# Kernel tuning notes

Measured on AMD Instinct MI355X. Metric: run time of the kernel, lower is better.

## Reference

```python
import jax, jax.numpy as jnp
import numpy as np


def _knn_idx(pts, k):
    # pts: [N, d] -> indices of k nearest neighbors (incl. self, loop=True) [N, k]
    sq = jnp.sum(pts * pts, axis=-1)
    d2 = sq[:, None] + sq[None, :] - 2.0 * (pts @ pts.T)  # [N, N] squared dists
    _, idx = jax.lax.top_k(-d2, k)  # k smallest distances
    return idx


def _graph_conv(x, nbr, Wr, br, Ws):
    # x: [B, N, d_in], nbr: [B, N, k]. GraphConv (aggr='add'):
    # out_i = W_rel @ sum_j x_j + b_rel + W_root @ x_i
    gathered = jax.vmap(lambda xb, ib: xb[ib])(x, nbr)  # [B, N, k, d_in]
    agg = gathered.sum(axis=2)                          # [B, N, d_in]
    return agg @ Wr.T + br + x @ Ws.T


def setup_inputs() -> dict:
    key = jax.random.key(0)
    ks = jax.random.split(key, 10)
    B, N, D, H = 16, 2048, 3, 128
    s = lambda fi, fo: (2.0 / (fi + fo)) ** 0.5
    return {
        "point_cloud": jax.random.normal(ks[0], (B, N, D), dtype=jnp.float32),
        "W1r": jax.random.normal(ks[1], (H, D), dtype=jnp.float32) * s(D, H),
        "b1": jnp.zeros((H,), dtype=jnp.float32),
        "W1s": jax.random.normal(ks[2], (H, D), dtype=jnp.float32) * s(D, H),
        "W2r": jax.random.normal(ks[3], (H, H), dtype=jnp.float32) * s(H, H),
        "b2": jnp.zeros((H,), dtype=jnp.float32),
        "W2s": jax.random.normal(ks[4], (H, H), dtype=jnp.float32) * s(H, H),
        "W3r": jax.random.normal(ks[5], (H, H), dtype=jnp.float32) * s(H, H),
        "b3": jnp.zeros((H,), dtype=jnp.float32),
        "W3s": jax.random.normal(ks[6], (H, H), dtype=jnp.float32) * s(H, H),
        "k": 16,
    }


def reference(point_cloud, W1r, b1, W1s, W2r, b2, W2s, W3r, b3, W3s, k):
    # knn graph per batch element (loop=True: self-loop included, d(i,i)=0)
    nbr = jax.vmap(lambda p: _knn_idx(p, k))(point_cloud)  # [B, N, k]
    x = jax.nn.relu(_graph_conv(point_cloud, nbr, W1r, b1, W1s))
    x = jax.nn.relu(_graph_conv(x, nbr, W2r, b2, W2s))
    x = _graph_conv(x, nbr, W3r, b3, W3s)
    return x  # [B, N, output_dim]
```

## Files before the change

kernel.cpp:

```cpp
#include <hip/hip_runtime.h>
#include <math.h>

#define NPTS 2048
#define BATCH 16
#define KNN 16
#define HID 128
#define RPB 8
#define CAP 128

typedef __attribute__((ext_vector_type(8))) short bf16x8;
typedef __attribute__((ext_vector_type(4))) float f32x4;

__device__ inline unsigned short f2bf(float f) {
    unsigned u = __float_as_uint(f);
    return (unsigned short)((u + 0x7FFFu + ((u >> 16) & 1u)) >> 16);
}
__device__ inline float bflo(unsigned v) { return __uint_as_float(v << 16); }
__device__ inline float bfhi(unsigned v) { return __uint_as_float(v & 0xFFFF0000u); }

__global__ __launch_bounds__(512) void knn_kernel(
    const float* __restrict__ pc, int* __restrict__ nbr,
    const float* __restrict__ W1r, const float* __restrict__ b1,
    const float* __restrict__ W1s, unsigned short* __restrict__ x1)
{
    __shared__ __align__(16) float4 pts[NPTS];
    __shared__ unsigned ckey[RPB][CAP];
    __shared__ unsigned cidx[RPB][CAP];

    const int b = blockIdx.x >> 8;
    const int rblk = blockIdx.x & 255;
    const float* p = pc + (size_t)b * NPTS * 3;

    for (int t = threadIdx.x; t < NPTS; t += 512) {
        float x = p[t * 3 + 0], y = p[t * 3 + 1], z = p[t * 3 + 2];
        pts[t] = make_float4(x, y, z, x * x + y * y + z * z);
    }
    __syncthreads();

    const int w = threadIdx.x >> 6;
    const int lane = threadIdx.x & 63;
    const int i = rblk * RPB + w;
    const float4 pi = pts[i];
    const float piw16 = pi.w + 16.0f;

    unsigned key[32];
    unsigned km = 0xFFFFFFFFu;
    #pragma unroll
    for (int t = 0; t < 32; ++t) {
        float4 c = pts[t * 64 + lane];
        float dot = fmaf(pi.x, c.x, fmaf(pi.y, c.y, pi.z * c.z));
        float d2 = fmaf(-2.0f, dot, piw16 + c.w);
        key[t] = __float_as_uint(d2);
        km = min(km, key[t]);
    }

    unsigned v = km;
    #pragma unroll
    for (int k = 2; k <= 64; k <<= 1) {
        #pragma unroll
        for (int j = k >> 1; j > 0; j >>= 1) {
            unsigned o = (unsigned)__shfl_xor((int)v, j, 64);
            bool sel = ((lane & k) == 0) == ((lane & j) == 0);
            v = sel ? min(v, o) : max(v, o);
        }
    }
    const unsigned T0 = (unsigned)__shfl((int)v, 15, 64);

    unsigned base = 0;
    #pragma unroll 1
    for (int t = 0; t < 32; ++t) {
        bool pred = key[t] <= T0;
        unsigned long long mask = __ballot(pred);
        if (mask) {
            unsigned prefix = __builtin_amdgcn_mbcnt_hi(
                (unsigned)(mask >> 32),
                __builtin_amdgcn_mbcnt_lo((unsigned)mask, 0));
            unsigned pos = base + prefix;
            if (pred && pos < CAP) {
                ckey[w][pos] = key[t];
                cidx[w][pos] = (unsigned)(t * 64 + lane);
            }
            base += (unsigned)__popcll(mask);
        }
    }
    __threadfence_block();
    const int m = (int)base;

    int* out = nbr + ((size_t)b * NPTS + i) * KNN;
    float ax = 0.f, ay = 0.f, az = 0.f;

    if (m <= CAP) {
        unsigned k0 = (lane < m) ? ckey[w][lane] : 0xFFFFFFFFu;
        unsigned k1 = (lane + 64 < m) ? ckey[w][lane + 64] : 0xFFFFFFFFu;
        int r0 = 0, r1 = 0;
        if (m <= 64) {
            #pragma unroll 1
            for (int jj = 0; jj < m; ++jj) {
                unsigned kj = ckey[w][jj];
                r0 += (kj < k0) || (kj == k0 && jj < lane);
            }
        } else {
            #pragma unroll 1
            for (int jj = 0; jj < m; ++jj) {
                unsigned kj = ckey[w][jj];
                r0 += (kj < k0) || (kj == k0 && jj < lane);
                r1 += (kj < k1) || (kj == k1 && jj < lane + 64);
            }
        }
        if (lane < m && r0 < KNN) {
            unsigned j = cidx[w][lane];
            out[r0] = (int)j;
            float4 q = pts[j]; ax += q.x; ay += q.y; az += q.z;
        }
        if (m > 64 && lane + 64 < m && r1 < KNN) {
            unsigned j = cidx[w][lane + 64];
            out[r1] = (int)j;
            float4 q = pts[j]; ax += q.x; ay += q.y; az += q.z;
        }
    } else {
        unsigned T = 0;
        #pragma unroll 1
        for (int bit = 31; bit >= 0; --bit) {
            unsigned trial = T | (1u << bit);
            int cnt = 0;
            #pragma unroll
            for (int t = 0; t < 32; ++t) cnt += (key[t] < trial);
            #pragma unroll
            for (int off = 32; off; off >>= 1)
                cnt += __shfl_xor(cnt, off, 64);
            if (cnt < KNN) T = trial;
        }
        unsigned bs = 0;
        #pragma unroll 1
        for (int t = 0; t < 32; ++t) {
            bool p1 = key[t] < T;
            unsigned long long mask = __ballot(p1);
            if (mask) {
                unsigned prefix = __builtin_amdgcn_mbcnt_hi(
                    (unsigned)(mask >> 32),
                    __builtin_amdgcn_mbcnt_lo((unsigned)mask, 0));
                if (p1) {
                    out[bs + prefix] = t * 64 + lane;
                    float4 q = pts[t * 64 + lane];
                    ax += q.x; ay += q.y; az += q.z;
                }
                bs += (unsigned)__popcll(mask);
            }
        }
        #pragma unroll 1
        for (int t = 0; t < 32 && bs < KNN; ++t) {
            bool p2 = key[t] == T;
            unsigned long long mask = __ballot(p2);
            if (mask) {
                unsigned prefix = __builtin_amdgcn_mbcnt_hi(
                    (unsigned)(mask >> 32),
                    __builtin_amdgcn_mbcnt_lo((unsigned)mask, 0));
                unsigned pos = bs + prefix;
                if (p2 && pos < KNN) {
                    out[pos] = t * 64 + lane;
                    float4 q = pts[t * 64 + lane];
                    ax += q.x; ay += q.y; az += q.z;
                }
                bs += (unsigned)__popcll(mask);
            }
        }
    }

    #pragma unroll
    for (int off = 32; off; off >>= 1) {
        ax += __shfl_xor(ax, off, 64);
        ay += __shfl_xor(ay, off, 64);
        az += __shfl_xor(az, off, 64);
    }

    unsigned short* xrow = x1 + ((size_t)b * NPTS + i) * HID;
    #pragma unroll
    for (int hh = 0; hh < 2; ++hh) {
        int h = lane + hh * 64;
        float acc = b1[h];
        acc += W1r[h * 3 + 0] * ax + W1r[h * 3 + 1] * ay + W1r[h * 3 + 2] * az;
        acc += W1s[h * 3 + 0] * pi.x + W1s[h * 3 + 1] * pi.y + W1s[h * 3 + 2] * pi.z;
        xrow[h] = f2bf(fmaxf(acc, 0.f));
    }
}

__global__ __launch_bounds__(256) void wcvt_kernel(
    const float* __restrict__ a, const float* __restrict__ b,
    const float* __restrict__ c, const float* __restrict__ d,
    unsigned short* __restrict__ out)
{
    int g = blockIdx.x * 256 + threadIdx.x;
    int m = g >> 14;
    const float* s = (m == 0) ? a : (m == 1) ? b : (m == 2) ? c : d;
    out[g] = f2bf(s[g & 16383]);
}

template <bool RELU, bool OUT_BF16>
__global__ __launch_bounds__(1024, 8) void conv_fused(
    const unsigned short* __restrict__ x, const int* __restrict__ nbr,
    const unsigned short* __restrict__ Wr, const unsigned short* __restrict__ Ws,
    const float* __restrict__ bias, void* __restrict__ outv)
{
    __shared__ __align__(16) unsigned short aggs[64][136];
    __shared__ int nbrs[64][17];
    const int p0 = blockIdx.x * 64;
    const int bt = p0 >> 11;
    const unsigned short* xb = x + ((size_t)bt << 11) * HID;

    {
        int e = threadIdx.x;
        nbrs[e >> 4][e & 15] = nbr[(size_t)p0 * KNN + e];
    }
    __syncthreads();

    {
        int c8 = threadIdx.x & 15, pt = threadIdx.x >> 4;
        const unsigned short* base = xb + c8 * 8;
        float s[8] = {0, 0, 0, 0, 0, 0, 0, 0};
        #pragma unroll
        for (int t = 0; t < KNN; ++t) {
            int j = nbrs[pt][t];
            uint4 v = *(const uint4*)(base + (size_t)j * HID);
            s[0] += bflo(v.x); s[1] += bfhi(v.x);
            s[2] += bflo(v.y); s[3] += bfhi(v.y);
            s[4] += bflo(v.z); s[5] += bfhi(v.z);
            s[6] += bflo(v.w); s[7] += bfhi(v.w);
        }
        uint4 ov;
        ov.x = (unsigned)f2bf(s[0]) | ((unsigned)f2bf(s[1]) << 16);
        ov.y = (unsigned)f2bf(s[2]) | ((unsigned)f2bf(s[3]) << 16);
        ov.z = (unsigned)f2bf(s[4]) | ((unsigned)f2bf(s[5]) << 16);
        ov.w = (unsigned)f2bf(s[6]) | ((unsigned)f2bf(s[7]) << 16);
        *(uint4*)&aggs[pt][c8 * 8] = ov;
    }
    __syncthreads();

    const int wv = threadIdx.x >> 6;
    const int lane = threadIdx.x & 63;
    const int ptw = (wv & 3) * 16;
    const int h0w = (wv >> 2) * 32;
    const int row = lane & 15;
    const int quad = lane >> 4;

    f32x4 acc[2];
    acc[0] = (f32x4){0, 0, 0, 0};
    acc[1] = (f32x4){0, 0, 0, 0};

    #pragma unroll
    for (int kc = 0; kc < 4; ++kc) {
        bf16x8 a0 = *(const bf16x8*)&aggs[ptw + row][quad * 8 + kc * 32];
        #pragma unroll
        for (int n = 0; n < 2; ++n) {
            bf16x8 bb = *(const bf16x8*)&Wr[(size_t)(h0w + n * 16 + row) * HID
                                            + quad * 8 + kc * 32];
            acc[n] = __builtin_amdgcn_mfma_f32_16x16x32_bf16(a0, bb, acc[n], 0, 0, 0);
        }
    }
    const unsigned short* xr0 = x + (size_t)(p0 + ptw + row) * HID + quad * 8;
    #pragma unroll
    for (int kc = 0; kc < 4; ++kc) {
        bf16x8 a0 = *(const bf16x8*)(xr0 + kc * 32);
        #pragma unroll
        for (int n = 0; n < 2; ++n) {
            bf16x8 bb = *(const bf16x8*)&Ws[(size_t)(h0w + n * 16 + row) * HID
                                            + quad * 8 + kc * 32];
            acc[n] = __builtin_amdgcn_mfma_f32_16x16x32_bf16(a0, bb, acc[n], 0, 0, 0);
        }
    }

    #pragma unroll
    for (int n = 0; n < 2; ++n) {
        float bh = bias[h0w + n * 16 + row];
        #pragma unroll
        for (int r = 0; r < 4; ++r) {
            int pp = p0 + ptw + quad * 4 + r;
            float vv = acc[n][r] + bh;
            if (RELU) vv = fmaxf(vv, 0.f);
            if (OUT_BF16)
                ((unsigned short*)outv)[(size_t)pp * HID + h0w + n * 16 + row] = f2bf(vv);
            else
                ((float*)outv)[(size_t)pp * HID + h0w + n * 16 + row] = vv;
        }
    }
}

extern "C" void kernel_launch(void* const* d_in, const int* in_sizes, int n_in,
                              void* d_out, int out_size, void* d_ws, size_t ws_size,
                              hipStream_t stream)
{
    const float* pc  = (const float*)d_in[0];
    const float* W1r = (const float*)d_in[1];
    const float* b1  = (const float*)d_in[2];
    const float* W1s = (const float*)d_in[3];
    const float* W2r = (const float*)d_in[4];
    const float* b2  = (const float*)d_in[5];
    const float* W2s = (const float*)d_in[6];
    const float* W3r = (const float*)d_in[7];
    const float* b3  = (const float*)d_in[8];
    const float* W3s = (const float*)d_in[9];
    float* out = (float*)d_out;

    char* ws = (char*)d_ws;
    const size_t MB = 1024 * 1024;
    int*            nbr = (int*)ws;
    unsigned short* x1  = (unsigned short*)(ws + 2 * MB);
    unsigned short* x2  = (unsigned short*)(ws + 2 * MB + 8388608);
    unsigned short* wbf = (unsigned short*)(ws + 2 * MB + 2 * 8388608);
    unsigned short* w2r = wbf;
    unsigned short* w2s = wbf + 16384;
    unsigned short* w3r = wbf + 32768;
    unsigned short* w3s = wbf + 49152;

    const int NPOINTS = BATCH * NPTS;

    wcvt_kernel<<<256, 256, 0, stream>>>(W2r, W2s, W3r, W3s, wbf);
    knn_kernel<<<NPOINTS / RPB, 512, 0, stream>>>(pc, nbr, W1r, b1, W1s, x1);

    conv_fused<true, true><<<NPOINTS / 64, 1024, 0, stream>>>(
        x1, nbr, w2r, w2s, b2, x2);
    conv_fused<false, false><<<NPOINTS / 64, 1024, 0, stream>>>(
        x2, nbr, w3r, w3s, b3, out);
}
```

Measured before the change: 185.1 us.

## Stage conv outputs through LDS for coalesced stores and halve block size

The conv kernel now runs 512 threads per block, each wave computing a 32x32 output tile (two row tiles) so every weight fragment load feeds two MFMAs. Results are first written to shared memory, which is reused for fp32 output, and then copied out with 16-byte vector stores along rows. Before, each lane wrote scalar values at a stride of one row. The change targets uncoalesced global stores and redundant weight loads. In exchange it adds two barriers and more LDS per block, which may lower occupancy.

```diff
diff --git a/kernel.cpp b/kernel.cpp
--- a/kernel.cpp
+++ b/kernel.cpp
@@ -196,25 +196,28 @@
 }
 
 template <bool RELU, bool OUT_BF16>
-__global__ __launch_bounds__(1024, 8) void conv_fused(
+__global__ __launch_bounds__(512) void conv_fused(
     const unsigned short* __restrict__ x, const int* __restrict__ nbr,
     const unsigned short* __restrict__ Wr, const unsigned short* __restrict__ Ws,
     const float* __restrict__ bias, void* __restrict__ outv)
 {
-    __shared__ __align__(16) unsigned short aggs[64][136];
+    __shared__ __align__(16) char smem[64 * 132 * 4];
     __shared__ int nbrs[64][17];
+    unsigned short (*aggs)[136] = (unsigned short (*)[136])smem;
+    float (*outs)[132] = (float (*)[132])smem;
+
     const int p0 = blockIdx.x * 64;
     const int bt = p0 >> 11;
     const unsigned short* xb = x + ((size_t)bt << 11) * HID;
 
-    {
-        int e = threadIdx.x;
+    for (int e = threadIdx.x; e < 64 * KNN; e += 512)
         nbrs[e >> 4][e & 15] = nbr[(size_t)p0 * KNN + e];
-    }
-    __syncthreads();
-
-    {
-        int c8 = threadIdx.x & 15, pt = threadIdx.x >> 4;
+    __syncthreads();
+
+    #pragma unroll
+    for (int it = 0; it < 2; ++it) {
+        int task = it * 512 + threadIdx.x;
+        int c8 = task & 15, pt = task >> 4;
         const unsigned short* base = xb + c8 * 8;
         float s[8] = {0, 0, 0, 0, 0, 0, 0, 0};
         #pragma unroll
@@ -237,49 +240,80 @@
 
     const int wv = threadIdx.x >> 6;
     const int lane = threadIdx.x & 63;
-    const int ptw = (wv & 3) * 16;
-    const int h0w = (wv >> 2) * 32;
+    const int ptw = (wv & 1) * 32;
+    const int h0w = (wv >> 1) * 32;
     const int row = lane & 15;
     const int quad = lane >> 4;
 
-    f32x4 acc[2];
-    acc[0] = (f32x4){0, 0, 0, 0};
-    acc[1] = (f32x4){0, 0, 0, 0};
+    f32x4 acc[2][2];
+    #pragma unroll
+    for (int i = 0; i < 2; ++i)
+        #pragma unroll
+        for (int n = 0; n < 2; ++n) acc[i][n] = (f32x4){0, 0, 0, 0};
 
     #pragma unroll
     for (int kc = 0; kc < 4; ++kc) {
         bf16x8 a0 = *(const bf16x8*)&aggs[ptw + row][quad * 8 + kc * 32];
+        bf16x8 a1 = *(const bf16x8*)&aggs[ptw + 16 + row][quad * 8 + kc * 32];
         #pragma unroll
         for (int n = 0; n < 2; ++n) {
             bf16x8 bb = *(const bf16x8*)&Wr[(size_t)(h0w + n * 16 + row) * HID
                                             + quad * 8 + kc * 32];
-            acc[n] = __builtin_amdgcn_mfma_f32_16x16x32_bf16(a0, bb, acc[n], 0, 0, 0);
+            acc[0][n] = __builtin_amdgcn_mfma_f32_16x16x32_bf16(a0, bb, acc[0][n], 0, 0, 0);
+            acc[1][n] = __builtin_amdgcn_mfma_f32_16x16x32_bf16(a1, bb, acc[1][n], 0, 0, 0);
         }
     }
     const unsigned short* xr0 = x + (size_t)(p0 + ptw + row) * HID + quad * 8;
+    const unsigned short* xr1 = xr0 + 16 * HID;
     #pragma unroll
     for (int kc = 0; kc < 4; ++kc) {
         bf16x8 a0 = *(const bf16x8*)(xr0 + kc * 32);
+        bf16x8 a1 = *(const bf16x8*)(xr1 + kc * 32);
         #pragma unroll
         for (int n = 0; n < 2; ++n) {
             bf16x8 bb = *(const bf16x8*)&Ws[(size_t)(h0w + n * 16 + row) * HID
                                             + quad * 8 + kc * 32];
-            acc[n] = __builtin_amdgcn_mfma_f32_16x16x32_bf16(a0, bb, acc[n], 0, 0, 0);
-        }
-    }
-
+            acc[0][n] = __builtin_amdgcn_mfma_f32_16x16x32_bf16(a0, bb, acc[0][n], 0, 0, 0);
+            acc[1][n] = __builtin_amdgcn_mfma_f32_16x16x32_bf16(a1, bb, acc[1][n], 0, 0, 0);
+        }
+    }
+
+    __syncthreads();
     #pragma unroll
     for (int n = 0; n < 2; ++n) {
         float bh = bias[h0w + n * 16 + row];
         #pragma unroll
-        for (int r = 0; r < 4; ++r) {
-            int pp = p0 + ptw + quad * 4 + r;
-            float vv = acc[n][r] + bh;
-            if (RELU) vv = fmaxf(vv, 0.f);
-            if (OUT_BF16)
-                ((unsigned short*)outv)[(size_t)pp * HID + h0w + n * 16 + row] = f2bf(vv);
-            else
-                ((float*)outv)[(size_t)pp * HID + h0w + n * 16 + row] = vv;
+        for (int i = 0; i < 2; ++i) {
+            #pragma unroll
+            for (int r = 0; r < 4; ++r) {
+                int pt = ptw + i * 16 + quad * 4 + r;
+                int hh = h0w + n * 16 + row;
+                float vv = acc[i][n][r] + bh;
+                if (RELU) vv = fmaxf(vv, 0.f);
+                if (OUT_BF16) aggs[pt][hh] = f2bf(vv);
+                else          outs[pt][hh] = vv;
+            }
+        }
+    }
+    __syncthreads();
+
+    if (OUT_BF16) {
+        unsigned short* o = (unsigned short*)outv;
+        #pragma unroll
+        for (int q = 0; q < 2; ++q) {
+            int task = q * 512 + threadIdx.x;
+            int rr = task >> 4, ch = task & 15;
+            *(uint4*)(o + (size_t)(p0 + rr) * HID + ch * 8) =
+                *(const uint4*)&aggs[rr][ch * 8];
+        }
+    } else {
+        float* o = (float*)outv;
+        #pragma unroll
+        for (int q = 0; q < 4; ++q) {
+            int task = q * 512 + threadIdx.x;
+            int rr = task >> 5, ch = task & 31;
+            *(float4*)(o + (size_t)(p0 + rr) * HID + ch * 4) =
+                *(const float4*)&outs[rr][ch * 4];
         }
     }
 }
@@ -316,8 +350,8 @@
     wcvt_kernel<<<256, 256, 0, stream>>>(W2r, W2s, W3r, W3s, wbf);
     knn_kernel<<<NPOINTS / RPB, 512, 0, stream>>>(pc, nbr, W1r, b1, W1s, x1);
 
-    conv_fused<true, true><<<NPOINTS / 64, 1024, 0, stream>>>(
+    conv_fused<true, true><<<NPOINTS / 64, 512, 0, stream>>>(
         x1, nbr, w2r, w2s, b2, x2);
-    conv_fused<false, false><<<NPOINTS / 64, 1024, 0, stream>>>(
+    conv_fused<false, false><<<NPOINTS / 64, 512, 0, stream>>>(
         x2, nbr, w3r, w3s, b3, out);
 }
```

New measurement: 174.4 us. 1.06x faster.
